# Kernel optimization log

Hardware: AMD Instinct MI355X
Metric: run time of the kernel (lower is better)

## Reference

```python
import jax, jax.numpy as jnp
import numpy as np


def _ragged_reverse(x, lengths):
    # x: [N, L, C]; flip the first `lengths[n]` steps of each sample, zero-fill the rest.
    N, L, C = x.shape
    t = jnp.arange(L, dtype=lengths.dtype)[None, :]          # [1, L]
    Ln = lengths[:, None]                                     # [N, 1]
    valid = t < Ln                                            # [N, L]
    idx = jnp.where(valid, Ln - 1 - t, 0)                     # [N, L]
    rev = jnp.take_along_axis(x, idx[:, :, None], axis=1)     # [N, L, C]
    return jnp.where(valid[:, :, None], rev, jnp.zeros((), x.dtype))


def _gru(xb, W_ih, W_hh, b_ih, b_hh):
    # xb: [B, L, C] -> outputs [B, L, H] (standard torch GRU cell math).
    B, L, C = xb.shape
    H = W_hh.shape[0]
    xw = xb @ W_ih + b_ih                                     # [B, L, 3H], input proj done once

    def step(h, xw_t):
        gh = h @ W_hh + b_hh                                  # [B, 3H]
        xr, xz, xn = jnp.split(xw_t, 3, axis=-1)
        hr, hz, hn = jnp.split(gh, 3, axis=-1)
        r = jax.nn.sigmoid(xr + hr)
        z = jax.nn.sigmoid(xz + hz)
        n = jnp.tanh(xn + r * hn)
        h_new = (1.0 - z) * n + z * h
        return h_new, h_new

    h0 = jnp.zeros((B, H), xb.dtype)
    _, ys = jax.lax.scan(step, h0, jnp.swapaxes(xw, 0, 1))    # ys: [L, B, H]
    return jnp.swapaxes(ys, 0, 1)                             # [B, L, H]


def reference(x, lengths, W_ih, W_hh, b_ih, b_hh):
    N, L, C = x.shape
    # to_bidirection: stack [forward; ragged-reversed] along batch -> [2N, L, C]
    rev = _ragged_reverse(x, lengths)
    xb = jnp.concatenate([x, rev], axis=0)
    out = _gru(xb, W_ih, W_hh, b_ih, b_hh)                    # [2N, L, H]
    # from_bidirection: split halves, concat on feature dim -> [N, L, 2H]
    return jnp.concatenate([out[:N], out[N:]], axis=2)


def setup_inputs() -> dict:
    key = jax.random.key(0)
    ks = jax.random.split(key, 6)
    N, L, C, H = 32, 2048, 64, 128
    s = 1.0 / np.sqrt(H)
    return {
        "x": jax.random.normal(ks[0], (N, L, C), dtype=jnp.float32),
        "lengths": jax.random.randint(ks[1], (N,), 1, L + 1, dtype=jnp.int32),
        "W_ih": jax.random.normal(ks[2], (C, 3 * H), dtype=jnp.float32) * s,
        "W_hh": jax.random.normal(ks[3], (H, 3 * H), dtype=jnp.float32) * s,
        "b_ih": jax.random.normal(ks[4], (3 * H,), dtype=jnp.float32) * s,
        "b_hh": jax.random.normal(ks[5], (3 * H,), dtype=jnp.float32) * s,
    }
```

## Files before the change

### kernel.cpp

```cpp
#include <hip/hip_runtime.h>

#define L_SEQ 2048
#define C_IN  64
#define HH    128
#define NSEQ  32
#define B2    64
#define G3    384
#define XW32  (C_IN / 2)
#define XTOT  (NSEQ * L_SEQ * XW32)
#define RSLOT 48
#define RG    130

typedef _Float16 f16x8 __attribute__((ext_vector_type(8)));
typedef float    f32x4 __attribute__((ext_vector_type(4)));
typedef _Float16 half2_t __attribute__((ext_vector_type(2)));

#define PINU(v) asm volatile("" : "+v"(v))
#define STEP_BARRIER() asm volatile("s_waitcnt lgkmcnt(0)\n\ts_barrier" ::: "memory")
#define MFMA16(a, b, c) __builtin_amdgcn_mfma_f32_16x16x32_f16((a), (b), (c), 0, 0, 0)

__device__ __forceinline__ float fdot2u(unsigned int a, unsigned int b, float c) {
    return __builtin_amdgcn_fdot2(__builtin_bit_cast(half2_t, a),
                                  __builtin_bit_cast(half2_t, b), c, false);
}
__device__ __forceinline__ unsigned int pack_h2(float a, float b) {
    half2_t t; t.x = (_Float16)a; t.y = (_Float16)b;
    return __builtin_bit_cast(unsigned int, t);
}
__device__ __forceinline__ float qadd1(float x) {
    int t = __builtin_amdgcn_update_dpp(0, __builtin_bit_cast(int, x),
                                        0xB1, 0xF, 0xF, true);
    return x + __builtin_bit_cast(float, t);
}
__device__ __forceinline__ float fast_sigmoid(float x) {
    float e = __builtin_amdgcn_exp2f(-1.4426950408889634f * x);
    return __builtin_amdgcn_rcpf(1.0f + e);
}
__device__ __forceinline__ float fast_tanh(float x) {
    float a = fabsf(x);
    float e = __builtin_amdgcn_exp2f(-2.8853900817779268f * a);
    float r = (1.0f - e) * __builtin_amdgcn_rcpf(1.0f + e);
    return copysignf(r, x);
}

__global__ __launch_bounds__(256)
void pack_x_kernel(const float* __restrict__ x, unsigned int* __restrict__ xh)
{
    const size_t i = (size_t)blockIdx.x * 256 + threadIdx.x;
    if (i < (size_t)XTOT) {
        const float2 v = ((const float2*)x)[i];
        xh[i] = pack_h2(v.x, v.y);
    }
    if (i < XW32) xh[(size_t)XTOT + i] = 0u;
}

__global__ __launch_bounds__(256) __attribute__((amdgpu_waves_per_eu(1, 1)))
void bigru_fused(const unsigned int* __restrict__ xh,
                 const int* __restrict__ lengths,
                 const float* __restrict__ W_ih, const float* __restrict__ W_hh,
                 const float* __restrict__ b_ih, const float* __restrict__ b_hh,
                 float* __restrict__ out)
{
    __shared__ unsigned int hbufu[2][64];
    __shared__ float ring[RSLOT][3][RG];

    const int tid = threadIdx.x;
    const int s   = blockIdx.x;
    const bool fwd = (s < NSEQ);
    const int  len = fwd ? L_SEQ : lengths[s - NSEQ];
    const unsigned int* __restrict__ xbase = xh + (size_t)(s % NSEQ) * L_SEQ * XW32;
    const unsigned int* __restrict__ zrow  = xh + (size_t)XTOT;

    const int j = tid >> 1;
    const int p = tid & 1;
    const int w  = tid >> 6;
    const int l  = tid & 63;
    const int lm = l & 15;
    const int lg = l >> 4;

    unsigned int wr[32], wz[32], wn[32];
    {
        const float* Wb = W_hh + (size_t)(64 * p) * G3;
#pragma unroll
        for (int k = 0; k < 32; ++k) {
            wr[k] = pack_h2(Wb[(2*k) * G3 + j],       Wb[(2*k+1) * G3 + j]);
            wz[k] = pack_h2(Wb[(2*k) * G3 + 128 + j], Wb[(2*k+1) * G3 + 128 + j]);
            wn[k] = pack_h2(Wb[(2*k) * G3 + 256 + j], Wb[(2*k+1) * G3 + 256 + j]);
        }
#pragma unroll
        for (int k = 0; k < 32; ++k) { PINU(wr[k]); PINU(wz[k]); PINU(wn[k]); }
    }
    float bn = b_hh[256 + j];
    PINU(bn);

    f16x8 Bx[3][2][2];
    float pbias[3][2];
#pragma unroll
    for (int g = 0; g < 3; ++g)
#pragma unroll
        for (int e = 0; e < 2; ++e) {
            const int gc = g * 128 + 32 * w + 16 * e + lm;
            pbias[g][e] = b_ih[gc] + ((g < 2) ? b_hh[gc] : 0.f);
#pragma unroll
            for (int kt = 0; kt < 2; ++kt) {
                f16x8 f;
#pragma unroll
                for (int i = 0; i < 8; ++i)
                    f[i] = (_Float16)W_ih[(kt * 32 + lg * 8 + i) * G3 + gc];
                Bx[g][e][kt] = f;
            }
        }

    uint4 AxP0, AxP1;
    auto loadA = [&](int rowBase) {
        const int row = rowBase + lm;
        const int src = fwd ? row : (len - 1 - row);
        const unsigned int* ptr = ((unsigned)src < (unsigned)L_SEQ)
                                ? (xbase + (size_t)src * XW32) : zrow;
        AxP0 = *(const uint4*)(ptr + lg * 4);
        AxP1 = *(const uint4*)(ptr + 16 + lg * 4);
    };
    auto produce = [&](int s0) {
        const f16x8 A0 = __builtin_bit_cast(f16x8, AxP0);
        const f16x8 A1 = __builtin_bit_cast(f16x8, AxP1);
#pragma unroll
        for (int g = 0; g < 3; ++g)
#pragma unroll
            for (int e = 0; e < 2; ++e) {
                f32x4 acc = {pbias[g][e], pbias[g][e], pbias[g][e], pbias[g][e]};
                acc = MFMA16(A0, Bx[g][e][0], acc);
                acc = MFMA16(A1, Bx[g][e][1], acc);
                const int colw = 32 * w + 16 * e + lm;
#pragma unroll
                for (int q = 0; q < 4; ++q)
                    ring[s0 + lg * 4 + q][g][colw] = acc[q];
            }
    };

    float hreg = 0.f;
    if (tid < 64) hbufu[0][tid] = 0u;

    loadA(0);  produce(0);
    loadA(16); produce(16);
    loadA(32);
    __syncthreads();

    float cr = ring[0][0][j], cz = ring[0][1][j], cn = ring[0][2][j];

    float* outbase = out + (size_t)(s % NSEQ) * L_SEQ * 256 + (fwd ? 0 : HH);
    int cur = 0;
    int slotN = 1;
    int s0 = 32;

    for (int t = 0; t < L_SEQ; ++t) {
        if ((t & 15) == 8) {
            if (t + 24 < L_SEQ) produce(s0);
            s0 += 16; if (s0 >= RSLOT) s0 -= RSLOT;
            if (t + 40 < L_SEQ) loadA(t + 40);
        }

        const float nr = ring[slotN][0][j];
        const float nz = ring[slotN][1][j];
        const float nn = ring[slotN][2][j];
        ++slotN; if (slotN == RSLOT) slotN = 0;

        float arA = 0.f, azA = 0.f, anA = 0.f;
        float arB = 0.f, azB = 0.f, anB = 0.f;
        const uint4* hb = (const uint4*)&hbufu[cur][p * 32];
#pragma unroll
        for (int i = 0; i < 4; ++i) {
            const uint4 hv = hb[i];
            arA = fdot2u(hv.x, wr[4*i+0], arA); arA = fdot2u(hv.y, wr[4*i+1], arA);
            arA = fdot2u(hv.z, wr[4*i+2], arA); arA = fdot2u(hv.w, wr[4*i+3], arA);
            azA = fdot2u(hv.x, wz[4*i+0], azA); azA = fdot2u(hv.y, wz[4*i+1], azA);
            azA = fdot2u(hv.z, wz[4*i+2], azA); azA = fdot2u(hv.w, wz[4*i+3], azA);
            anA = fdot2u(hv.x, wn[4*i+0], anA); anA = fdot2u(hv.y, wn[4*i+1], anA);
            anA = fdot2u(hv.z, wn[4*i+2], anA); anA = fdot2u(hv.w, wn[4*i+3], anA);
        }
#pragma unroll
        for (int i = 4; i < 8; ++i) {
            const uint4 hv = hb[i];
            arB = fdot2u(hv.x, wr[4*i+0], arB); arB = fdot2u(hv.y, wr[4*i+1], arB);
            arB = fdot2u(hv.z, wr[4*i+2], arB); arB = fdot2u(hv.w, wr[4*i+3], arB);
            azB = fdot2u(hv.x, wz[4*i+0], azB); azB = fdot2u(hv.y, wz[4*i+1], azB);
            azB = fdot2u(hv.z, wz[4*i+2], azB); azB = fdot2u(hv.w, wz[4*i+3], azB);
            anB = fdot2u(hv.x, wn[4*i+0], anB); anB = fdot2u(hv.y, wn[4*i+1], anB);
            anB = fdot2u(hv.z, wn[4*i+2], anB); anB = fdot2u(hv.w, wn[4*i+3], anB);
        }
        float ar = arA + arB, az = azA + azB, an = anA + anB;
        ar = qadd1(ar); az = qadd1(az); an = qadd1(an);

        const float r = fast_sigmoid(cr + ar);
        const float z = fast_sigmoid(cz + az);
        const float n = fast_tanh(cn + r * (an + bn));
        const float hnew = z * (hreg - n) + n;
        hreg = hnew;

        if (p == 0) {
            ((_Float16*)&hbufu[cur ^ 1][0])[j] = (_Float16)hnew;
            outbase[(size_t)t * 256 + j] = hnew;
        }
        STEP_BARRIER();
        cur ^= 1;
        cr = nr; cz = nz; cn = nn;
    }
}

extern "C" void kernel_launch(void* const* d_in, const int* in_sizes, int n_in,
                              void* d_out, int out_size, void* d_ws, size_t ws_size,
                              hipStream_t stream) {
    const float* x       = (const float*)d_in[0];
    const int*   lengths = (const int*)  d_in[1];
    const float* W_ih    = (const float*)d_in[2];
    const float* W_hh    = (const float*)d_in[3];
    const float* b_ih    = (const float*)d_in[4];
    const float* b_hh    = (const float*)d_in[5];
    float* out = (float*)d_out;

    unsigned int* xh = (unsigned int*)d_ws;

    pack_x_kernel<<<dim3((XTOT + 255) / 256), dim3(256), 0, stream>>>(x, xh);
    bigru_fused<<<dim3(B2), dim3(256), 0, stream>>>(
        xh, lengths, W_ih, W_hh, b_ih, b_hh, out);
}
```

Before: 945.3 us.

## Process forward and reversed sequences in one block to interleave recurrences

Each block now runs both the forward and the ragged-reversed GRU recurrence for one sample, so the grid drops from 64 to 32 blocks. Two independent dependency chains per step are meant to hide the latency of the dot products, the transcendentals and the per-step barrier, and it halves the number of barriers across the whole job. The input-projection ring is reorganised to a gate-interleaved layout with 32 slots per direction, with production staggered at two phases. The cost is roughly double the work per step in each block and more register pressure, using half as many CUs.

```diff
diff --git a/kernel.cpp b/kernel.cpp
--- a/kernel.cpp
+++ b/kernel.cpp
@@ -4,12 +4,11 @@
 #define C_IN  64
 #define HH    128
 #define NSEQ  32
-#define B2    64
 #define G3    384
 #define XW32  (C_IN / 2)
 #define XTOT  (NSEQ * L_SEQ * XW32)
-#define RSLOT 48
-#define RG    130
+#define RSLOT 32
+#define RCOL  3
 
 typedef _Float16 f16x8 __attribute__((ext_vector_type(8)));
 typedef float    f32x4 __attribute__((ext_vector_type(4)));
@@ -55,28 +54,23 @@
 }
 
 __global__ __launch_bounds__(256) __attribute__((amdgpu_waves_per_eu(1, 1)))
-void bigru_fused(const unsigned int* __restrict__ xh,
-                 const int* __restrict__ lengths,
-                 const float* __restrict__ W_ih, const float* __restrict__ W_hh,
-                 const float* __restrict__ b_ih, const float* __restrict__ b_hh,
-                 float* __restrict__ out)
+void bigru_dual(const unsigned int* __restrict__ xh,
+                const int* __restrict__ lengths,
+                const float* __restrict__ W_ih, const float* __restrict__ W_hh,
+                const float* __restrict__ b_ih, const float* __restrict__ b_hh,
+                float* __restrict__ out)
 {
-    __shared__ unsigned int hbufu[2][64];
-    __shared__ float ring[RSLOT][3][RG];
+    __shared__ float ring[2][RSLOT][HH * RCOL];
+    __shared__ unsigned int hbufu[2][2][64];
 
     const int tid = threadIdx.x;
-    const int s   = blockIdx.x;
-    const bool fwd = (s < NSEQ);
-    const int  len = fwd ? L_SEQ : lengths[s - NSEQ];
-    const unsigned int* __restrict__ xbase = xh + (size_t)(s % NSEQ) * L_SEQ * XW32;
-    const unsigned int* __restrict__ zrow  = xh + (size_t)XTOT;
-
-    const int j = tid >> 1;
-    const int p = tid & 1;
-    const int w  = tid >> 6;
-    const int l  = tid & 63;
-    const int lm = l & 15;
-    const int lg = l >> 4;
+    const int b   = blockIdx.x;
+    const int j   = tid >> 1;
+    const int p   = tid & 1;
+    const int w   = tid >> 6;
+    const int l   = tid & 63;
+    const int lm  = l & 15;
+    const int lg  = l >> 4;
 
     unsigned int wr[32], wz[32], wn[32];
     {
@@ -111,18 +105,22 @@
             }
         }
 
-    uint4 AxP0, AxP1;
-    auto loadA = [&](int rowBase) {
+    const unsigned int* __restrict__ xbase = xh + (size_t)b * L_SEQ * XW32;
+    const unsigned int* __restrict__ zrow  = xh + (size_t)XTOT;
+    const int len = lengths[b];
+
+    uint4 AxF0, AxF1, AxR0, AxR1;
+    auto loadA = [&](bool rev, int rowBase, uint4& A0, uint4& A1) {
         const int row = rowBase + lm;
-        const int src = fwd ? row : (len - 1 - row);
+        const int src = rev ? (len - 1 - row) : row;
         const unsigned int* ptr = ((unsigned)src < (unsigned)L_SEQ)
                                 ? (xbase + (size_t)src * XW32) : zrow;
-        AxP0 = *(const uint4*)(ptr + lg * 4);
-        AxP1 = *(const uint4*)(ptr + 16 + lg * 4);
+        A0 = *(const uint4*)(ptr + lg * 4);
+        A1 = *(const uint4*)(ptr + 16 + lg * 4);
     };
-    auto produce = [&](int s0) {
-        const f16x8 A0 = __builtin_bit_cast(f16x8, AxP0);
-        const f16x8 A1 = __builtin_bit_cast(f16x8, AxP1);
+    auto produce = [&](int seq, int s0, uint4 P0, uint4 P1) {
+        const f16x8 A0 = __builtin_bit_cast(f16x8, P0);
+        const f16x8 A1 = __builtin_bit_cast(f16x8, P1);
 #pragma unroll
         for (int g = 0; g < 3; ++g)
 #pragma unroll
@@ -133,76 +131,93 @@
                 const int colw = 32 * w + 16 * e + lm;
 #pragma unroll
                 for (int q = 0; q < 4; ++q)
-                    ring[s0 + lg * 4 + q][g][colw] = acc[q];
+                    ring[seq][s0 + lg * 4 + q][colw * RCOL + g] = acc[q];
             }
     };
 
-    float hreg = 0.f;
-    if (tid < 64) hbufu[0][tid] = 0u;
-
-    loadA(0);  produce(0);
-    loadA(16); produce(16);
-    loadA(32);
+    loadA(false, 0, AxF0, AxF1);  produce(0, 0, AxF0, AxF1);
+    loadA(true,  0, AxR0, AxR1);  produce(1, 0, AxR0, AxR1);
+    loadA(false, 16, AxF0, AxF1);
+
+    float hF = 0.f, hR = 0.f;
+    if (tid < 64) { hbufu[0][0][tid] = 0u; hbufu[1][0][tid] = 0u; }
     __syncthreads();
 
-    float cr = ring[0][0][j], cz = ring[0][1][j], cn = ring[0][2][j];
-
-    float* outbase = out + (size_t)(s % NSEQ) * L_SEQ * 256 + (fwd ? 0 : HH);
+    float crF = ring[0][0][j * RCOL + 0], czF = ring[0][0][j * RCOL + 1],
+          cnF = ring[0][0][j * RCOL + 2];
+    float crR = ring[1][0][j * RCOL + 0], czR = ring[1][0][j * RCOL + 1],
+          cnR = ring[1][0][j * RCOL + 2];
+
+    float* op = out + (size_t)b * L_SEQ * 256;
     int cur = 0;
-    int slotN = 1;
-    int s0 = 32;
 
     for (int t = 0; t < L_SEQ; ++t) {
-        if ((t & 15) == 8) {
-            if (t + 24 < L_SEQ) produce(s0);
-            s0 += 16; if (s0 >= RSLOT) s0 -= RSLOT;
-            if (t + 40 < L_SEQ) loadA(t + 40);
-        }
-
-        const float nr = ring[slotN][0][j];
-        const float nz = ring[slotN][1][j];
-        const float nn = ring[slotN][2][j];
-        ++slotN; if (slotN == RSLOT) slotN = 0;
-
-        float arA = 0.f, azA = 0.f, anA = 0.f;
-        float arB = 0.f, azB = 0.f, anB = 0.f;
-        const uint4* hb = (const uint4*)&hbufu[cur][p * 32];
-#pragma unroll
-        for (int i = 0; i < 4; ++i) {
-            const uint4 hv = hb[i];
-            arA = fdot2u(hv.x, wr[4*i+0], arA); arA = fdot2u(hv.y, wr[4*i+1], arA);
-            arA = fdot2u(hv.z, wr[4*i+2], arA); arA = fdot2u(hv.w, wr[4*i+3], arA);
-            azA = fdot2u(hv.x, wz[4*i+0], azA); azA = fdot2u(hv.y, wz[4*i+1], azA);
-            azA = fdot2u(hv.z, wz[4*i+2], azA); azA = fdot2u(hv.w, wz[4*i+3], azA);
-            anA = fdot2u(hv.x, wn[4*i+0], anA); anA = fdot2u(hv.y, wn[4*i+1], anA);
-            anA = fdot2u(hv.z, wn[4*i+2], anA); anA = fdot2u(hv.w, wn[4*i+3], anA);
-        }
-#pragma unroll
-        for (int i = 4; i < 8; ++i) {
-            const uint4 hv = hb[i];
-            arB = fdot2u(hv.x, wr[4*i+0], arB); arB = fdot2u(hv.y, wr[4*i+1], arB);
-            arB = fdot2u(hv.z, wr[4*i+2], arB); arB = fdot2u(hv.w, wr[4*i+3], arB);
-            azB = fdot2u(hv.x, wz[4*i+0], azB); azB = fdot2u(hv.y, wz[4*i+1], azB);
-            azB = fdot2u(hv.z, wz[4*i+2], azB); azB = fdot2u(hv.w, wz[4*i+3], azB);
-            anB = fdot2u(hv.x, wn[4*i+0], anB); anB = fdot2u(hv.y, wn[4*i+1], anB);
-            anB = fdot2u(hv.z, wn[4*i+2], anB); anB = fdot2u(hv.w, wn[4*i+3], anB);
-        }
-        float ar = arA + arB, az = azA + azB, an = anA + anB;
-        ar = qadd1(ar); az = qadd1(az); an = qadd1(an);
-
-        const float r = fast_sigmoid(cr + ar);
-        const float z = fast_sigmoid(cz + az);
-        const float n = fast_tanh(cn + r * (an + bn));
-        const float hnew = z * (hreg - n) + n;
-        hreg = hnew;
+        const int ph = t & 15;
+        if (ph == 0) {
+            produce(0, (t + 16) & (RSLOT - 1), AxF0, AxF1);
+            loadA(true, t + 16, AxR0, AxR1);
+        } else if (ph == 8) {
+            produce(1, (t + 8) & (RSLOT - 1), AxR0, AxR1);
+            loadA(false, t + 24, AxF0, AxF1);
+        }
+
+        const int sl = (t + 1) & (RSLOT - 1);
+        const float nrF = ring[0][sl][j * RCOL + 0];
+        const float nzF = ring[0][sl][j * RCOL + 1];
+        const float nnF = ring[0][sl][j * RCOL + 2];
+        const float nrR = ring[1][sl][j * RCOL + 0];
+        const float nzR = ring[1][sl][j * RCOL + 1];
+        const float nnR = ring[1][sl][j * RCOL + 2];
+
+        float arF = 0.f, azF = 0.f, anF = 0.f;
+        float arR = 0.f, azR = 0.f, anR = 0.f;
+        const uint4* hbF = (const uint4*)&hbufu[0][cur][p * 32];
+        const uint4* hbR = (const uint4*)&hbufu[1][cur][p * 32];
+#pragma unroll
+        for (int i = 0; i < 8; ++i) {
+            const uint4 hv = hbF[i];
+            arF = fdot2u(hv.x, wr[4*i+0], arF); arF = fdot2u(hv.y, wr[4*i+1], arF);
+            arF = fdot2u(hv.z, wr[4*i+2], arF); arF = fdot2u(hv.w, wr[4*i+3], arF);
+            azF = fdot2u(hv.x, wz[4*i+0], azF); azF = fdot2u(hv.y, wz[4*i+1], azF);
+            azF = fdot2u(hv.z, wz[4*i+2], azF); azF = fdot2u(hv.w, wz[4*i+3], azF);
+            anF = fdot2u(hv.x, wn[4*i+0], anF); anF = fdot2u(hv.y, wn[4*i+1], anF);
+            anF = fdot2u(hv.z, wn[4*i+2], anF); anF = fdot2u(hv.w, wn[4*i+3], anF);
+        }
+#pragma unroll
+        for (int i = 0; i < 8; ++i) {
+            const uint4 hv = hbR[i];
+            arR = fdot2u(hv.x, wr[4*i+0], arR); arR = fdot2u(hv.y, wr[4*i+1], arR);
+            arR = fdot2u(hv.z, wr[4*i+2], arR); arR = fdot2u(hv.w, wr[4*i+3], arR);
+            azR = fdot2u(hv.x, wz[4*i+0], azR); azR = fdot2u(hv.y, wz[4*i+1], azR);
+            azR = fdot2u(hv.z, wz[4*i+2], azR); azR = fdot2u(hv.w, wz[4*i+3], azR);
+            anR = fdot2u(hv.x, wn[4*i+0], anR); anR = fdot2u(hv.y, wn[4*i+1], anR);
+            anR = fdot2u(hv.z, wn[4*i+2], anR); anR = fdot2u(hv.w, wn[4*i+3], anR);
+        }
+        arF = qadd1(arF); azF = qadd1(azF); anF = qadd1(anF);
+        arR = qadd1(arR); azR = qadd1(azR); anR = qadd1(anR);
+
+        const float rF = fast_sigmoid(crF + arF);
+        const float zF = fast_sigmoid(czF + azF);
+        const float nF = fast_tanh(cnF + rF * (anF + bn));
+        const float hFn = zF * (hF - nF) + nF;
+        hF = hFn;
+        const float rR = fast_sigmoid(crR + arR);
+        const float zR = fast_sigmoid(czR + azR);
+        const float nR = fast_tanh(cnR + rR * (anR + bn));
+        const float hRn = zR * (hR - nR) + nR;
+        hR = hRn;
 
         if (p == 0) {
-            ((_Float16*)&hbufu[cur ^ 1][0])[j] = (_Float16)hnew;
-            outbase[(size_t)t * 256 + j] = hnew;
+            ((_Float16*)&hbufu[0][cur ^ 1][0])[j] = (_Float16)hFn;
+            ((_Float16*)&hbufu[1][cur ^ 1][0])[j] = (_Float16)hRn;
+            float* o = op + (size_t)t * 256;
+            o[j]        = hFn;
+            o[128 + j]  = hRn;
         }
         STEP_BARRIER();
         cur ^= 1;
-        cr = nr; cz = nz; cn = nn;
+        crF = nrF; czF = nzF; cnF = nnF;
+        crR = nrR; czR = nzR; cnR = nnR;
     }
 }
 
@@ -220,6 +235,6 @@
     unsigned int* xh = (unsigned int*)d_ws;
 
     pack_x_kernel<<<dim3((XTOT + 255) / 256), dim3(256), 0, stream>>>(x, xh);
-    bigru_fused<<<dim3(B2), dim3(256), 0, stream>>>(
+    bigru_dual<<<dim3(NSEQ), dim3(256), 0, stream>>>(
         xh, lengths, W_ih, W_hh, b_ih, b_hh, out);
 }
```

Measured after the change: 1.628 ms. 1.72x slower.
